# Kernel optimization log

Measured on AMD Instinct MI355X. Metric: run time of the kernel, lower is better.

Reference implementation:

```python
import jax, jax.numpy as jnp
import numpy as np

NPOINT, NSAMPLE, RADIUS, EPS = 128, 32, 0.4, 1e-5
C_IN, C_MID, C_OUT = 256, 256, 256


def setup_inputs() -> dict:
    key = jax.random.key(0)
    ks = jax.random.split(key, 6)
    B, N = 8, 16384
    xyz = jax.random.uniform(ks[0], (B, N, 3), dtype=jnp.float32)
    feats = jax.random.normal(ks[1], (B, N, C_IN), dtype=jnp.float32)
    # SharedMLP: Conv2d 1x1 (no bias, followed by BN) layers 259->256, 256->256
    w1 = jax.random.normal(ks[2], (C_MID, C_IN + 3), dtype=jnp.float32) * 0.05
    w2 = jax.random.normal(ks[3], (C_OUT, C_MID), dtype=jnp.float32) * 0.05
    gamma1 = jnp.ones((C_MID,), jnp.float32); beta1 = jnp.zeros((C_MID,), jnp.float32)
    mean1 = jnp.zeros((C_MID,), jnp.float32); var1 = jnp.ones((C_MID,), jnp.float32)
    gamma2 = jnp.ones((C_OUT,), jnp.float32); beta2 = jnp.zeros((C_OUT,), jnp.float32)
    mean2 = jnp.zeros((C_OUT,), jnp.float32); var2 = jnp.ones((C_OUT,), jnp.float32)
    return {"xyz": xyz, "proposal_features": feats,
            "w1": w1, "gamma1": gamma1, "beta1": beta1, "mean1": mean1, "var1": var1,
            "w2": w2, "gamma2": gamma2, "beta2": beta2, "mean2": mean2, "var2": var2}


def fps(xyz, npoint):
    # Farthest point sampling, CUDA-kernel-faithful: starts at index 0.
    B, N, _ = xyz.shape
    def step(carry, _):
        dist, far = carry
        centroid = jnp.take_along_axis(xyz, far[:, None, None], axis=1)  # [B,1,3]
        d = jnp.sum((xyz - centroid) ** 2, axis=-1)                      # [B,N]
        dist = jnp.minimum(dist, d)
        return (dist, jnp.argmax(dist, axis=-1).astype(jnp.int32)), far
    init = (jnp.full((B, N), 1e10, xyz.dtype), jnp.zeros((B,), jnp.int32))
    _, inds = jax.lax.scan(step, init, None, length=npoint)
    return inds.T  # [B, npoint]


def ball_query(xyz, new_xyz, radius, nsample):
    # First-nsample-in-order points within radius, padded with the first hit.
    B, N, _ = xyz.shape
    d2 = jnp.sum((new_xyz[:, :, None, :] - xyz[:, None, :, :]) ** 2, axis=-1)  # [B,S,N]
    keys = jnp.where(d2 < radius * radius, jnp.arange(N, dtype=jnp.int32), N)
    idx = -jax.lax.top_k(-keys, nsample)[0]  # smallest indices, ascending
    idx = jnp.where(idx < N, idx, idx[..., :1])  # pad invalid with first hit
    return jnp.clip(idx, 0, N - 1)


def gather_points(pts_bnc, idx):
    # pts_bnc [B,N,C], idx [B,S,K] -> [B,S,K,C]
    B, S, K = idx.shape
    flat = jnp.take_along_axis(pts_bnc, idx.reshape(B, S * K)[:, :, None], axis=1)
    return flat.reshape(B, S, K, pts_bnc.shape[-1])


def bn_relu(x, gamma, beta, mean, var):
    return jax.nn.relu((x - mean) * jax.lax.rsqrt(var + EPS) * gamma + beta)


def reference(xyz, proposal_features, w1, gamma1, beta1, mean1, var1,
              w2, gamma2, beta2, mean2, var2):
    # proposal_features arrives as [B, N, C]; torch module permutes to [B, C, N]
    # (we keep channels-last internally, equivalent math).
    inds = fps(xyz, NPOINT)                                   # [B,128]
    new_xyz = jnp.take_along_axis(xyz, inds[:, :, None], axis=1)  # [B,128,3]
    idx = ball_query(xyz, new_xyz, RADIUS, NSAMPLE)           # [B,128,32]
    g_xyz = gather_points(xyz, idx) - new_xyz[:, :, None, :]  # [B,128,32,3]
    g_feat = gather_points(proposal_features, idx)            # [B,128,32,256]
    x = jnp.concatenate([g_xyz, g_feat], axis=-1)             # [B,128,32,259]
    h = bn_relu(jnp.einsum('bskc,oc->bsko', x, w1), gamma1, beta1, mean1, var1)
    h = bn_relu(jnp.einsum('bskc,oc->bsko', h, w2), gamma2, beta2, mean2, var2)
    new_features = jnp.max(h, axis=2)                         # [B,128,256]
    return jnp.transpose(new_features, (0, 2, 1))             # [B,256,128]
```

## Files before the change

### kernel.cpp

```cpp
#include <hip/hip_runtime.h>
#include <hip/hip_bf16.h>
#include <cstdint>
#include <cstddef>

#define NB      8
#define NPTS    16384
#define NPOINT  128
#define NSAMPLE 32
#define CIN     256
#define CMID    256
#define COUT    256
#define KDIM    259
#define KPAD    288
#define XS_STRIDE 296
#define HS_STRIDE 264

typedef __attribute__((ext_vector_type(8))) short bf16x8;
typedef __attribute__((ext_vector_type(4))) short s16x4;
typedef __attribute__((ext_vector_type(4))) float f32x4;
typedef __attribute__((ext_vector_type(2))) float f32x2;

__device__ __forceinline__ short f2bf(float f) {
  unsigned u = __float_as_uint(f);
  u += 0x7fffu + ((u >> 16) & 1u);
  return (short)(u >> 16);
}

template <int CTRL, int RMASK>
__device__ __forceinline__ unsigned long long dpp_umax_step(unsigned long long v) {
  int lo = (int)(unsigned)(v & 0xffffffffull);
  int hi = (int)(unsigned)(v >> 32);
  int nlo = __builtin_amdgcn_update_dpp(lo, lo, CTRL, RMASK, 0xf, false);
  int nhi = __builtin_amdgcn_update_dpp(hi, hi, CTRL, RMASK, 0xf, false);
  unsigned long long o = ((unsigned long long)(unsigned)nhi << 32) | (unsigned)nlo;
  return o > v ? o : v;
}

#define FPS_T 512
#define FPS_W (FPS_T / 64)
#define FPS_P (NPTS / FPS_T)
#define FPS_PH (FPS_P / 2)

__global__ __launch_bounds__(FPS_T) __attribute__((amdgpu_waves_per_eu(2, 2)))
void fps_kernel(const float* __restrict__ xyz, int* __restrict__ inds) {
#pragma clang fp contract(off)
  const int b = blockIdx.x;
  const int t = threadIdx.x;
  const int lane = t & 63, w = t >> 6;
  const float* xb = xyz + (size_t)b * NPTS * 3;

  f32x2 px[FPS_PH], py[FPS_PH], pz[FPS_PH], dv[FPS_PH];
#pragma unroll
  for (int i = 0; i < FPS_PH; ++i) {
    const int j0 = t + (2 * i) * FPS_T;
    const int j1 = j0 + FPS_T;
    px[i] = (f32x2){xb[j0 * 3 + 0], xb[j1 * 3 + 0]};
    py[i] = (f32x2){xb[j0 * 3 + 1], xb[j1 * 3 + 1]};
    pz[i] = (f32x2){xb[j0 * 3 + 2], xb[j1 * 3 + 2]};
    dv[i] = (f32x2){1e10f, 1e10f};
  }
#pragma unroll
  for (int i = 0; i < FPS_PH; ++i) {
    asm volatile("" : "+v"(px[i]), "+v"(py[i]), "+v"(pz[i]), "+v"(dv[i]));
  }

  __shared__ unsigned long long s_pack[2][FPS_W];
  __shared__ float swx[2][FPS_W], swy[2][FPS_W], swz[2][FPS_W];

  int far = 0;
  float cx = xb[0], cy = xb[1], cz = xb[2];

  for (int it = 0; it < NPOINT; ++it) {
    if (t == 0) inds[b * NPOINT + it] = far;
    const f32x2 vcx = {cx, cx}, vcy = {cy, cy}, vcz = {cz, cz};
    f32x2 best2 = {-1.0f, -1.0f};
#pragma unroll
    for (int i = 0; i < FPS_PH; ++i) {
      f32x2 dx = px[i] - vcx;
      f32x2 dy = py[i] - vcy;
      f32x2 dz = pz[i] - vcz;
      f32x2 d2 = (dx * dx + dy * dy) + dz * dz;
      f32x2 dm = {fminf(dv[i].x, d2.x), fminf(dv[i].y, d2.y)};
      dv[i] = dm;
      best2 = (f32x2){fmaxf(best2.x, dm.x), fmaxf(best2.y, dm.y)};
    }
    const float best = fmaxf(best2.x, best2.y);
    int sl = 0;
#pragma unroll
    for (int i = FPS_PH - 1; i >= 0; --i) {
      if (dv[i].y == best) sl = 2 * i + 1;
      if (dv[i].x == best) sl = 2 * i;
    }
    const int bi = t + (sl << 9);

    unsigned long long pk = ((unsigned long long)__float_as_uint(best) << 17)
                          | ((unsigned long long)(unsigned)(NPTS - 1 - bi) << 3)
                          | (unsigned long long)w;

    pk = dpp_umax_step<0x111, 0xf>(pk);
    pk = dpp_umax_step<0x112, 0xf>(pk);
    pk = dpp_umax_step<0x114, 0xf>(pk);
    pk = dpp_umax_step<0x118, 0xf>(pk);
    pk = dpp_umax_step<0x142, 0xa>(pk);
    pk = dpp_umax_step<0x143, 0xc>(pk);
    const unsigned wlo = (unsigned)__builtin_amdgcn_readlane((int)(unsigned)(pk & 0xffffffffull), 63);
    const unsigned whi = (unsigned)__builtin_amdgcn_readlane((int)(unsigned)(pk >> 32), 63);
    const unsigned long long wavepk = ((unsigned long long)whi << 32) | wlo;
    const int wbi = (NPTS - 1) - (int)((wavepk >> 3) & (unsigned long long)(NPTS - 1));

    const int slot = __builtin_amdgcn_readfirstlane(wbi >> 9);
    float bx = 0.f, by = 0.f, bz = 0.f;
#define CASE_SLOT(k) \
    case (2 * (k)):     bx = px[k].x; by = py[k].x; bz = pz[k].x; break; \
    case (2 * (k) + 1): bx = px[k].y; by = py[k].y; bz = pz[k].y; break;
    switch (slot) {
      CASE_SLOT(0)  CASE_SLOT(1)  CASE_SLOT(2)  CASE_SLOT(3)
      CASE_SLOT(4)  CASE_SLOT(5)  CASE_SLOT(6)  CASE_SLOT(7)
      CASE_SLOT(8)  CASE_SLOT(9)  CASE_SLOT(10) CASE_SLOT(11)
      CASE_SLOT(12) CASE_SLOT(13) CASE_SLOT(14) CASE_SLOT(15)
      default: break;
    }
#undef CASE_SLOT

    const int par = it & 1;
    if (lane == (wbi & 63)) {
      s_pack[par][w] = wavepk;
      swx[par][w] = bx; swy[par][w] = by; swz[par][w] = bz;
    }
    __syncthreads();
    unsigned long long pm = s_pack[par][lane & 7];
    pm = dpp_umax_step<0x124, 0xf>(pm);
    pm = dpp_umax_step<0x4E, 0xf>(pm);
    pm = dpp_umax_step<0xB1, 0xf>(pm);
    const int wi = (int)(pm & 7ull);
    far = (NPTS - 1) - (int)((pm >> 3) & (unsigned long long)(NPTS - 1));
    cx = swx[par][wi]; cy = swy[par][wi]; cz = swz[par][wi];
  }
}

__global__ __launch_bounds__(256) void prep_kernel(
    const float* __restrict__ w1, const float* __restrict__ g1, const float* __restrict__ be1,
    const float* __restrict__ m1, const float* __restrict__ v1,
    const float* __restrict__ w2, const float* __restrict__ g2, const float* __restrict__ be2,
    const float* __restrict__ m2, const float* __restrict__ v2,
    short* __restrict__ w1b, short* __restrict__ w2b,
    float* __restrict__ b1, float* __restrict__ b2) {
  int i = blockIdx.x * 256 + threadIdx.x;
  if (i < CMID * KPAD) {
    int oc = i / KPAD, p = i - oc * KPAD;
    float a = g1[oc] * rsqrtf(v1[oc] + 1e-5f);
    float val;
    if (p < 256)      val = w1[oc * KDIM + 3 + p] * a;
    else if (p < KDIM) val = w1[oc * KDIM + (p - 256)] * a;
    else              val = 0.0f;
    w1b[i] = f2bf(val);
    if (p == 0) b1[oc] = be1[oc] - m1[oc] * a;
  }
  if (i < COUT * CMID) {
    int oc = i >> 8, c = i & 255;
    float a = g2[oc] * rsqrtf(v2[oc] + 1e-5f);
    w2b[i] = f2bf(w2[oc * CMID + c] * a);
    if (c == 0) b2[oc] = be2[oc] - m2[oc] * a;
  }
}

__global__ __launch_bounds__(256) void mlp_kernel(
    const float* __restrict__ xyz, const float* __restrict__ feats,
    const int* __restrict__ inds,
    const short* __restrict__ w1b, const short* __restrict__ w2b,
    const float* __restrict__ b1, const float* __restrict__ b2,
    float* __restrict__ out) {
  const int g   = blockIdx.x;
  const int bb  = g >> 7, s = g & 127;
  const int tid = threadIdx.x;
  const int wave = tid >> 6, lane = tid & 63;
  const int lrow = lane & 15, quad = lane >> 4;

  __shared__ short Xs[32 * XS_STRIDE];
  __shared__ short Hs[32 * HS_STRIDE];
  __shared__ int   sj[NSAMPLE];

  const float* xb = xyz + (size_t)bb * NPTS * 3;
  const int ind = inds[bb * NPOINT + s];
  const float cx = xb[ind * 3 + 0], cy = xb[ind * 3 + 1], cz = xb[ind * 3 + 2];

  if (wave == 0) {
    const float R2 = (float)(0.4 * 0.4);
    int total = 0;
    int first_hit = 0;
    bool have_first = false;
    for (int base = 0; base < NPTS && total < NSAMPLE; base += 64) {
      const int j = base + lane;
      float dx = __fsub_rn(xb[j * 3 + 0], cx);
      float dy = __fsub_rn(xb[j * 3 + 1], cy);
      float dz = __fsub_rn(xb[j * 3 + 2], cz);
      float d2 = __fadd_rn(__fadd_rn(__fmul_rn(dx, dx), __fmul_rn(dy, dy)), __fmul_rn(dz, dz));
      bool hit = d2 < R2;
      unsigned long long m = __ballot(hit);
      if (!have_first && m) { first_hit = base + (int)__builtin_ctzll(m); have_first = true; }
      int pos = total + (int)__popcll(m & ((1ull << lane) - 1ull));
      if (hit && pos < NSAMPLE) sj[pos] = j;
      total += (int)__popcll(m);
    }
    for (int p = total + lane; p < NSAMPLE; p += 64) sj[p] = first_hit;
  }
  __syncthreads();

  const float4* f4 = (const float4*)(feats + (size_t)bb * NPTS * CIN);
  for (int u = tid; u < 32 * 64; u += 256) {
    const int r = u >> 6, q = u & 63;
    float4 v = f4[(size_t)sj[r] * 64 + q];
    s16x4 pv = {f2bf(v.x), f2bf(v.y), f2bf(v.z), f2bf(v.w)};
    *(s16x4*)(&Xs[r * XS_STRIDE + 4 * q]) = pv;
  }
  for (int u = tid; u < 32 * 32; u += 256) {
    const int r = u >> 5, c = u & 31;
    const int j = sj[r];
    float val = 0.0f;
    if (c == 0)      val = xb[j * 3 + 0] - cx;
    else if (c == 1) val = xb[j * 3 + 1] - cy;
    else if (c == 2) val = xb[j * 3 + 2] - cz;
    Xs[r * XS_STRIDE + 256 + c] = f2bf(val);
  }
  __syncthreads();

  const int nw = wave * 64;
  f32x4 acc[4][2];
#pragma unroll
  for (int nt = 0; nt < 4; ++nt)
#pragma unroll
    for (int mt = 0; mt < 2; ++mt) acc[nt][mt] = (f32x4){0.f, 0.f, 0.f, 0.f};

  for (int ks = 0; ks < 9; ++ks) {
    const int ko = ks * 32 + quad * 8;
    bf16x8 a0 = *(const bf16x8*)(&Xs[lrow * XS_STRIDE + ko]);
    bf16x8 a1 = *(const bf16x8*)(&Xs[(lrow + 16) * XS_STRIDE + ko]);
#pragma unroll
    for (int nt = 0; nt < 4; ++nt) {
      const int oc = nw + nt * 16 + lrow;
      bf16x8 bf = *(const bf16x8*)(w1b + oc * KPAD + ko);
      acc[nt][0] = __builtin_amdgcn_mfma_f32_16x16x32_bf16(a0, bf, acc[nt][0], 0, 0, 0);
      acc[nt][1] = __builtin_amdgcn_mfma_f32_16x16x32_bf16(a1, bf, acc[nt][1], 0, 0, 0);
    }
  }

#pragma unroll
  for (int nt = 0; nt < 4; ++nt) {
    const int oc = nw + nt * 16 + lrow;
    const float bias = b1[oc];
#pragma unroll
    for (int mt = 0; mt < 2; ++mt) {
#pragma unroll
      for (int r = 0; r < 4; ++r) {
        int row = mt * 16 + quad * 4 + r;
        float h = fmaxf(acc[nt][mt][r] + bias, 0.0f);
        Hs[row * HS_STRIDE + oc] = f2bf(h);
      }
    }
  }
  __syncthreads();

#pragma unroll
  for (int nt = 0; nt < 4; ++nt)
#pragma unroll
    for (int mt = 0; mt < 2; ++mt) acc[nt][mt] = (f32x4){0.f, 0.f, 0.f, 0.f};

  for (int ks = 0; ks < 8; ++ks) {
    const int ko = ks * 32 + quad * 8;
    bf16x8 a0 = *(const bf16x8*)(&Hs[lrow * HS_STRIDE + ko]);
    bf16x8 a1 = *(const bf16x8*)(&Hs[(lrow + 16) * HS_STRIDE + ko]);
#pragma unroll
    for (int nt = 0; nt < 4; ++nt) {
      const int oc = nw + nt * 16 + lrow;
      bf16x8 bf = *(const bf16x8*)(w2b + oc * CMID + ko);
      acc[nt][0] = __builtin_amdgcn_mfma_f32_16x16x32_bf16(a0, bf, acc[nt][0], 0, 0, 0);
      acc[nt][1] = __builtin_amdgcn_mfma_f32_16x16x32_bf16(a1, bf, acc[nt][1], 0, 0, 0);
    }
  }

#pragma unroll
  for (int nt = 0; nt < 4; ++nt) {
    const int oc = nw + nt * 16 + lrow;
    const float bias = b2[oc];
    float v = -3.4e38f;
#pragma unroll
    for (int mt = 0; mt < 2; ++mt) {
      f32x4 a = acc[nt][mt];
      v = fmaxf(v, fmaxf(fmaxf(a[0], a[1]), fmaxf(a[2], a[3])));
    }
    v = fmaxf(v + bias, 0.0f);
    v = fmaxf(v, __shfl_xor(v, 16, 64));
    v = fmaxf(v, __shfl_xor(v, 32, 64));
    if (lane < 16) out[((size_t)bb * COUT + oc) * NPOINT + s] = v;
  }
}

extern "C" void kernel_launch(void* const* d_in, const int* in_sizes, int n_in,
                              void* d_out, int out_size, void* d_ws, size_t ws_size,
                              hipStream_t stream) {
  const float* xyz   = (const float*)d_in[0];
  const float* feats = (const float*)d_in[1];
  const float* w1    = (const float*)d_in[2];
  const float* g1    = (const float*)d_in[3];
  const float* be1   = (const float*)d_in[4];
  const float* m1    = (const float*)d_in[5];
  const float* v1    = (const float*)d_in[6];
  const float* w2    = (const float*)d_in[7];
  const float* g2    = (const float*)d_in[8];
  const float* be2   = (const float*)d_in[9];
  const float* m2    = (const float*)d_in[10];
  const float* v2    = (const float*)d_in[11];
  float* out = (float*)d_out;

  char* ws = (char*)d_ws;
  int*   inds = (int*)(ws);
  short* w1b  = (short*)(ws + 135168);
  short* w2b  = (short*)(ws + 282624);
  float* b1   = (float*)(ws + 413696);
  float* b2   = (float*)(ws + 414720);

  prep_kernel<<<288, 256, 0, stream>>>(w1, g1, be1, m1, v1, w2, g2, be2, m2, v2,
                                       w1b, w2b, b1, b2);
  fps_kernel<<<NB, FPS_T, 0, stream>>>(xyz, inds);
  mlp_kernel<<<NB * NPOINT, 256, 0, stream>>>(xyz, feats, inds, w1b, w2b, b1, b2, out);
}
```

Before: 439.7 us.

## Fuse FPS and MLP into one persistent launch with per-centroid flag handoff

Merges the farthest-point-sampling kernel and the grouped MLP kernel into a single launch. The first NB blocks run FPS and publish each centroid index with a release-flag, while the remaining blocks spin on their flag and start ball query plus MLP as soon as their centroid is ready. This lets MLP work overlap the long serial FPS loop instead of waiting for it to finish. MLP blocks now run 512 threads, so each wave covers half as many output channels. The spin-wait depends on FPS blocks being scheduled ahead of or alongside consumers, and there is a spin timeout that could yield wrong results if exceeded.

```diff
diff --git a/kernel.cpp b/kernel.cpp
--- a/kernel.cpp
+++ b/kernel.cpp
@@ -42,146 +42,133 @@
 #define FPS_PH (FPS_P / 2)
 
 __global__ __launch_bounds__(FPS_T) __attribute__((amdgpu_waves_per_eu(2, 2)))
-void fps_kernel(const float* __restrict__ xyz, int* __restrict__ inds) {
+void fused_kernel(const float* __restrict__ xyz, const float* __restrict__ feats,
+                  int* __restrict__ inds, unsigned* __restrict__ flags,
+                  const short* __restrict__ w1b, const short* __restrict__ w2b,
+                  const float* __restrict__ b1, const float* __restrict__ b2,
+                  float* __restrict__ out) {
 #pragma clang fp contract(off)
-  const int b = blockIdx.x;
-  const int t = threadIdx.x;
-  const int lane = t & 63, w = t >> 6;
-  const float* xb = xyz + (size_t)b * NPTS * 3;
-
-  f32x2 px[FPS_PH], py[FPS_PH], pz[FPS_PH], dv[FPS_PH];
-#pragma unroll
-  for (int i = 0; i < FPS_PH; ++i) {
-    const int j0 = t + (2 * i) * FPS_T;
-    const int j1 = j0 + FPS_T;
-    px[i] = (f32x2){xb[j0 * 3 + 0], xb[j1 * 3 + 0]};
-    py[i] = (f32x2){xb[j0 * 3 + 1], xb[j1 * 3 + 1]};
-    pz[i] = (f32x2){xb[j0 * 3 + 2], xb[j1 * 3 + 2]};
-    dv[i] = (f32x2){1e10f, 1e10f};
-  }
-#pragma unroll
-  for (int i = 0; i < FPS_PH; ++i) {
-    asm volatile("" : "+v"(px[i]), "+v"(py[i]), "+v"(pz[i]), "+v"(dv[i]));
-  }
-
-  __shared__ unsigned long long s_pack[2][FPS_W];
-  __shared__ float swx[2][FPS_W], swy[2][FPS_W], swz[2][FPS_W];
-
-  int far = 0;
-  float cx = xb[0], cy = xb[1], cz = xb[2];
-
-  for (int it = 0; it < NPOINT; ++it) {
-    if (t == 0) inds[b * NPOINT + it] = far;
-    const f32x2 vcx = {cx, cx}, vcy = {cy, cy}, vcz = {cz, cz};
-    f32x2 best2 = {-1.0f, -1.0f};
-#pragma unroll
-    for (int i = 0; i < FPS_PH; ++i) {
-      f32x2 dx = px[i] - vcx;
-      f32x2 dy = py[i] - vcy;
-      f32x2 dz = pz[i] - vcz;
-      f32x2 d2 = (dx * dx + dy * dy) + dz * dz;
-      f32x2 dm = {fminf(dv[i].x, d2.x), fminf(dv[i].y, d2.y)};
-      dv[i] = dm;
-      best2 = (f32x2){fmaxf(best2.x, dm.x), fmaxf(best2.y, dm.y)};
-    }
-    const float best = fmaxf(best2.x, best2.y);
-    int sl = 0;
-#pragma unroll
-    for (int i = FPS_PH - 1; i >= 0; --i) {
-      if (dv[i].y == best) sl = 2 * i + 1;
-      if (dv[i].x == best) sl = 2 * i;
-    }
-    const int bi = t + (sl << 9);
-
-    unsigned long long pk = ((unsigned long long)__float_as_uint(best) << 17)
-                          | ((unsigned long long)(unsigned)(NPTS - 1 - bi) << 3)
-                          | (unsigned long long)w;
-
-    pk = dpp_umax_step<0x111, 0xf>(pk);
-    pk = dpp_umax_step<0x112, 0xf>(pk);
-    pk = dpp_umax_step<0x114, 0xf>(pk);
-    pk = dpp_umax_step<0x118, 0xf>(pk);
-    pk = dpp_umax_step<0x142, 0xa>(pk);
-    pk = dpp_umax_step<0x143, 0xc>(pk);
-    const unsigned wlo = (unsigned)__builtin_amdgcn_readlane((int)(unsigned)(pk & 0xffffffffull), 63);
-    const unsigned whi = (unsigned)__builtin_amdgcn_readlane((int)(unsigned)(pk >> 32), 63);
-    const unsigned long long wavepk = ((unsigned long long)whi << 32) | wlo;
-    const int wbi = (NPTS - 1) - (int)((wavepk >> 3) & (unsigned long long)(NPTS - 1));
-
-    const int slot = __builtin_amdgcn_readfirstlane(wbi >> 9);
-    float bx = 0.f, by = 0.f, bz = 0.f;
-#define CASE_SLOT(k) \
-    case (2 * (k)):     bx = px[k].x; by = py[k].x; bz = pz[k].x; break; \
-    case (2 * (k) + 1): bx = px[k].y; by = py[k].y; bz = pz[k].y; break;
-    switch (slot) {
-      CASE_SLOT(0)  CASE_SLOT(1)  CASE_SLOT(2)  CASE_SLOT(3)
-      CASE_SLOT(4)  CASE_SLOT(5)  CASE_SLOT(6)  CASE_SLOT(7)
-      CASE_SLOT(8)  CASE_SLOT(9)  CASE_SLOT(10) CASE_SLOT(11)
-      CASE_SLOT(12) CASE_SLOT(13) CASE_SLOT(14) CASE_SLOT(15)
-      default: break;
-    }
-#undef CASE_SLOT
-
-    const int par = it & 1;
-    if (lane == (wbi & 63)) {
-      s_pack[par][w] = wavepk;
-      swx[par][w] = bx; swy[par][w] = by; swz[par][w] = bz;
-    }
-    __syncthreads();
-    unsigned long long pm = s_pack[par][lane & 7];
-    pm = dpp_umax_step<0x124, 0xf>(pm);
-    pm = dpp_umax_step<0x4E, 0xf>(pm);
-    pm = dpp_umax_step<0xB1, 0xf>(pm);
-    const int wi = (int)(pm & 7ull);
-    far = (NPTS - 1) - (int)((pm >> 3) & (unsigned long long)(NPTS - 1));
-    cx = swx[par][wi]; cy = swy[par][wi]; cz = swz[par][wi];
-  }
-}
-
-__global__ __launch_bounds__(256) void prep_kernel(
-    const float* __restrict__ w1, const float* __restrict__ g1, const float* __restrict__ be1,
-    const float* __restrict__ m1, const float* __restrict__ v1,
-    const float* __restrict__ w2, const float* __restrict__ g2, const float* __restrict__ be2,
-    const float* __restrict__ m2, const float* __restrict__ v2,
-    short* __restrict__ w1b, short* __restrict__ w2b,
-    float* __restrict__ b1, float* __restrict__ b2) {
-  int i = blockIdx.x * 256 + threadIdx.x;
-  if (i < CMID * KPAD) {
-    int oc = i / KPAD, p = i - oc * KPAD;
-    float a = g1[oc] * rsqrtf(v1[oc] + 1e-5f);
-    float val;
-    if (p < 256)      val = w1[oc * KDIM + 3 + p] * a;
-    else if (p < KDIM) val = w1[oc * KDIM + (p - 256)] * a;
-    else              val = 0.0f;
-    w1b[i] = f2bf(val);
-    if (p == 0) b1[oc] = be1[oc] - m1[oc] * a;
-  }
-  if (i < COUT * CMID) {
-    int oc = i >> 8, c = i & 255;
-    float a = g2[oc] * rsqrtf(v2[oc] + 1e-5f);
-    w2b[i] = f2bf(w2[oc * CMID + c] * a);
-    if (c == 0) b2[oc] = be2[oc] - m2[oc] * a;
-  }
-}
-
-__global__ __launch_bounds__(256) void mlp_kernel(
-    const float* __restrict__ xyz, const float* __restrict__ feats,
-    const int* __restrict__ inds,
-    const short* __restrict__ w1b, const short* __restrict__ w2b,
-    const float* __restrict__ b1, const float* __restrict__ b2,
-    float* __restrict__ out) {
-  const int g   = blockIdx.x;
-  const int bb  = g >> 7, s = g & 127;
   const int tid = threadIdx.x;
-  const int wave = tid >> 6, lane = tid & 63;
-  const int lrow = lane & 15, quad = lane >> 4;
+  const int lane = tid & 63;
 
   __shared__ short Xs[32 * XS_STRIDE];
   __shared__ short Hs[32 * HS_STRIDE];
   __shared__ int   sj[NSAMPLE];
-
+  __shared__ int   s_ind;
+  __shared__ unsigned long long s_pack[2][FPS_W];
+  __shared__ float swx[2][FPS_W], swy[2][FPS_W], swz[2][FPS_W];
+
+  if (blockIdx.x < NB) {
+    const int b = blockIdx.x;
+    const int t = tid, w = t >> 6;
+    const float* xb = xyz + (size_t)b * NPTS * 3;
+
+    f32x2 px[FPS_PH], py[FPS_PH], pz[FPS_PH], dv[FPS_PH];
+#pragma unroll
+    for (int i = 0; i < FPS_PH; ++i) {
+      const int j0 = t + (2 * i) * FPS_T;
+      const int j1 = j0 + FPS_T;
+      px[i] = (f32x2){xb[j0 * 3 + 0], xb[j1 * 3 + 0]};
+      py[i] = (f32x2){xb[j0 * 3 + 1], xb[j1 * 3 + 1]};
+      pz[i] = (f32x2){xb[j0 * 3 + 2], xb[j1 * 3 + 2]};
+      dv[i] = (f32x2){1e10f, 1e10f};
+    }
+#pragma unroll
+    for (int i = 0; i < FPS_PH; ++i) {
+      asm volatile("" : "+v"(px[i]), "+v"(py[i]), "+v"(pz[i]), "+v"(dv[i]));
+    }
+
+    int far = 0;
+    float cx = xb[0], cy = xb[1], cz = xb[2];
+
+    for (int it = 0; it < NPOINT; ++it) {
+      if (t == 0) {
+        inds[b * NPOINT + it] = far;
+        __hip_atomic_store(&flags[b * NPOINT + it], 1u, __ATOMIC_RELEASE,
+                           __HIP_MEMORY_SCOPE_AGENT);
+      }
+      const f32x2 vcx = {cx, cx}, vcy = {cy, cy}, vcz = {cz, cz};
+      f32x2 best2 = {-1.0f, -1.0f};
+#pragma unroll
+      for (int i = 0; i < FPS_PH; ++i) {
+        f32x2 dx = px[i] - vcx;
+        f32x2 dy = py[i] - vcy;
+        f32x2 dz = pz[i] - vcz;
+        f32x2 d2 = (dx * dx + dy * dy) + dz * dz;
+        f32x2 dm = {fminf(dv[i].x, d2.x), fminf(dv[i].y, d2.y)};
+        dv[i] = dm;
+        best2 = (f32x2){fmaxf(best2.x, dm.x), fmaxf(best2.y, dm.y)};
+      }
+      const float best = fmaxf(best2.x, best2.y);
+      int sl = 0;
+#pragma unroll
+      for (int i = FPS_PH - 1; i >= 0; --i) {
+        if (dv[i].y == best) sl = 2 * i + 1;
+        if (dv[i].x == best) sl = 2 * i;
+      }
+      const int bi = t + (sl << 9);
+
+      unsigned long long pk = ((unsigned long long)__float_as_uint(best) << 17)
+                            | ((unsigned long long)(unsigned)(NPTS - 1 - bi) << 3)
+                            | (unsigned long long)w;
+      pk = dpp_umax_step<0x111, 0xf>(pk);
+      pk = dpp_umax_step<0x112, 0xf>(pk);
+      pk = dpp_umax_step<0x114, 0xf>(pk);
+      pk = dpp_umax_step<0x118, 0xf>(pk);
+      pk = dpp_umax_step<0x142, 0xa>(pk);
+      pk = dpp_umax_step<0x143, 0xc>(pk);
+      const unsigned wlo = (unsigned)__builtin_amdgcn_readlane((int)(unsigned)(pk & 0xffffffffull), 63);
+      const unsigned whi = (unsigned)__builtin_amdgcn_readlane((int)(unsigned)(pk >> 32), 63);
+      const unsigned long long wavepk = ((unsigned long long)whi << 32) | wlo;
+      const int wbi = (NPTS - 1) - (int)((wavepk >> 3) & (unsigned long long)(NPTS - 1));
+
+      const int slot = __builtin_amdgcn_readfirstlane(wbi >> 9);
+      float bx = 0.f, by = 0.f, bz = 0.f;
+#define CASE_SLOT(k) \
+      case (2 * (k)):     bx = px[k].x; by = py[k].x; bz = pz[k].x; break; \
+      case (2 * (k) + 1): bx = px[k].y; by = py[k].y; bz = pz[k].y; break;
+      switch (slot) {
+        CASE_SLOT(0)  CASE_SLOT(1)  CASE_SLOT(2)  CASE_SLOT(3)
+        CASE_SLOT(4)  CASE_SLOT(5)  CASE_SLOT(6)  CASE_SLOT(7)
+        CASE_SLOT(8)  CASE_SLOT(9)  CASE_SLOT(10) CASE_SLOT(11)
+        CASE_SLOT(12) CASE_SLOT(13) CASE_SLOT(14) CASE_SLOT(15)
+        default: break;
+      }
+#undef CASE_SLOT
+
+      const int par = it & 1;
+      if (lane == (wbi & 63)) {
+        s_pack[par][w] = wavepk;
+        swx[par][w] = bx; swy[par][w] = by; swz[par][w] = bz;
+      }
+      __syncthreads();
+      unsigned long long pm = s_pack[par][lane & 7];
+      pm = dpp_umax_step<0x124, 0xf>(pm);
+      pm = dpp_umax_step<0x4E, 0xf>(pm);
+      pm = dpp_umax_step<0xB1, 0xf>(pm);
+      const int wi = (int)(pm & 7ull);
+      far = (NPTS - 1) - (int)((pm >> 3) & (unsigned long long)(NPTS - 1));
+      cx = swx[par][wi]; cy = swy[par][wi]; cz = swz[par][wi];
+    }
+    return;
+  }
+
+  const int g  = blockIdx.x - NB;
+  const int bb = g >> 7, s = g & 127;
+  const int wave = tid >> 6;
+  const int lrow = lane & 15, quad = lane >> 4;
   const float* xb = xyz + (size_t)bb * NPTS * 3;
-  const int ind = inds[bb * NPOINT + s];
+
+  if (tid == 0) {
+    unsigned spins = 0;
+    while (__hip_atomic_load(&flags[g], __ATOMIC_ACQUIRE,
+                             __HIP_MEMORY_SCOPE_AGENT) == 0u) {
+      if (++spins > (1u << 23)) break;
+    }
+    s_ind = __hip_atomic_load(&inds[g], __ATOMIC_RELAXED, __HIP_MEMORY_SCOPE_AGENT);
+  }
+  __syncthreads();
+  const int ind = s_ind;
   const float cx = xb[ind * 3 + 0], cy = xb[ind * 3 + 1], cz = xb[ind * 3 + 2];
 
   if (wave == 0) {
@@ -207,13 +194,13 @@
   __syncthreads();
 
   const float4* f4 = (const float4*)(feats + (size_t)bb * NPTS * CIN);
-  for (int u = tid; u < 32 * 64; u += 256) {
+  for (int u = tid; u < 32 * 64; u += FPS_T) {
     const int r = u >> 6, q = u & 63;
     float4 v = f4[(size_t)sj[r] * 64 + q];
     s16x4 pv = {f2bf(v.x), f2bf(v.y), f2bf(v.z), f2bf(v.w)};
     *(s16x4*)(&Xs[r * XS_STRIDE + 4 * q]) = pv;
   }
-  for (int u = tid; u < 32 * 32; u += 256) {
+  for (int u = tid; u < 32 * 32; u += FPS_T) {
     const int r = u >> 5, c = u & 31;
     const int j = sj[r];
     float val = 0.0f;
@@ -224,10 +211,10 @@
   }
   __syncthreads();
 
-  const int nw = wave * 64;
-  f32x4 acc[4][2];
-#pragma unroll
-  for (int nt = 0; nt < 4; ++nt)
+  const int nw = wave * 32;
+  f32x4 acc[2][2];
+#pragma unroll
+  for (int nt = 0; nt < 2; ++nt)
 #pragma unroll
     for (int mt = 0; mt < 2; ++mt) acc[nt][mt] = (f32x4){0.f, 0.f, 0.f, 0.f};
 
@@ -236,7 +223,7 @@
     bf16x8 a0 = *(const bf16x8*)(&Xs[lrow * XS_STRIDE + ko]);
     bf16x8 a1 = *(const bf16x8*)(&Xs[(lrow + 16) * XS_STRIDE + ko]);
 #pragma unroll
-    for (int nt = 0; nt < 4; ++nt) {
+    for (int nt = 0; nt < 2; ++nt) {
       const int oc = nw + nt * 16 + lrow;
       bf16x8 bf = *(const bf16x8*)(w1b + oc * KPAD + ko);
       acc[nt][0] = __builtin_amdgcn_mfma_f32_16x16x32_bf16(a0, bf, acc[nt][0], 0, 0, 0);
@@ -245,7 +232,7 @@
   }
 
 #pragma unroll
-  for (int nt = 0; nt < 4; ++nt) {
+  for (int nt = 0; nt < 2; ++nt) {
     const int oc = nw + nt * 16 + lrow;
     const float bias = b1[oc];
 #pragma unroll
@@ -261,7 +248,7 @@
   __syncthreads();
 
 #pragma unroll
-  for (int nt = 0; nt < 4; ++nt)
+  for (int nt = 0; nt < 2; ++nt)
 #pragma unroll
     for (int mt = 0; mt < 2; ++mt) acc[nt][mt] = (f32x4){0.f, 0.f, 0.f, 0.f};
 
@@ -270,7 +257,7 @@
     bf16x8 a0 = *(const bf16x8*)(&Hs[lrow * HS_STRIDE + ko]);
     bf16x8 a1 = *(const bf16x8*)(&Hs[(lrow + 16) * HS_STRIDE + ko]);
 #pragma unroll
-    for (int nt = 0; nt < 4; ++nt) {
+    for (int nt = 0; nt < 2; ++nt) {
       const int oc = nw + nt * 16 + lrow;
       bf16x8 bf = *(const bf16x8*)(w2b + oc * CMID + ko);
       acc[nt][0] = __builtin_amdgcn_mfma_f32_16x16x32_bf16(a0, bf, acc[nt][0], 0, 0, 0);
@@ -279,7 +266,7 @@
   }
 
 #pragma unroll
-  for (int nt = 0; nt < 4; ++nt) {
+  for (int nt = 0; nt < 2; ++nt) {
     const int oc = nw + nt * 16 + lrow;
     const float bias = b2[oc];
     float v = -3.4e38f;
@@ -292,6 +279,34 @@
     v = fmaxf(v, __shfl_xor(v, 16, 64));
     v = fmaxf(v, __shfl_xor(v, 32, 64));
     if (lane < 16) out[((size_t)bb * COUT + oc) * NPOINT + s] = v;
+  }
+}
+
+__global__ __launch_bounds__(256) void prep_kernel(
+    const float* __restrict__ w1, const float* __restrict__ g1, const float* __restrict__ be1,
+    const float* __restrict__ m1, const float* __restrict__ v1,
+    const float* __restrict__ w2, const float* __restrict__ g2, const float* __restrict__ be2,
+    const float* __restrict__ m2, const float* __restrict__ v2,
+    short* __restrict__ w1b, short* __restrict__ w2b,
+    float* __restrict__ b1, float* __restrict__ b2,
+    unsigned* __restrict__ flags) {
+  int i = blockIdx.x * 256 + threadIdx.x;
+  if (i < NB * NPOINT) flags[i] = 0u;
+  if (i < CMID * KPAD) {
+    int oc = i / KPAD, p = i - oc * KPAD;
+    float a = g1[oc] * rsqrtf(v1[oc] + 1e-5f);
+    float val;
+    if (p < 256)      val = w1[oc * KDIM + 3 + p] * a;
+    else if (p < KDIM) val = w1[oc * KDIM + (p - 256)] * a;
+    else              val = 0.0f;
+    w1b[i] = f2bf(val);
+    if (p == 0) b1[oc] = be1[oc] - m1[oc] * a;
+  }
+  if (i < COUT * CMID) {
+    int oc = i >> 8, c = i & 255;
+    float a = g2[oc] * rsqrtf(v2[oc] + 1e-5f);
+    w2b[i] = f2bf(w2[oc * CMID + c] * a);
+    if (c == 0) b2[oc] = be2[oc] - m2[oc] * a;
   }
 }
 
@@ -313,14 +328,15 @@
   float* out = (float*)d_out;
 
   char* ws = (char*)d_ws;
-  int*   inds = (int*)(ws);
-  short* w1b  = (short*)(ws + 135168);
-  short* w2b  = (short*)(ws + 282624);
-  float* b1   = (float*)(ws + 413696);
-  float* b2   = (float*)(ws + 414720);
+  int*      inds  = (int*)(ws);
+  short*    w1b   = (short*)(ws + 135168);
+  short*    w2b   = (short*)(ws + 282624);
+  float*    b1    = (float*)(ws + 413696);
+  float*    b2    = (float*)(ws + 414720);
+  unsigned* flags = (unsigned*)(ws + 415744);
 
   prep_kernel<<<288, 256, 0, stream>>>(w1, g1, be1, m1, v1, w2, g2, be2, m2, v2,
-                                       w1b, w2b, b1, b2);
-  fps_kernel<<<NB, FPS_T, 0, stream>>>(xyz, inds);
-  mlp_kernel<<<NB * NPOINT, 256, 0, stream>>>(xyz, feats, inds, w1b, w2b, b1, b2, out);
-}
+                                       w1b, w2b, b1, b2, flags);
+  fused_kernel<<<NB + NB * NPOINT, FPS_T, 0, stream>>>(xyz, feats, inds, flags,
+                                                       w1b, w2b, b1, b2, out);
+}
```

Result: slower. 594.8 us (+35.3%).
